# Kernel optimization log

Hardware: AMD Instinct MI355X
Metric: run time of the kernel (lower is better)

The kernel has to match this reference:

```python
import jax, jax.numpy as jnp
import numpy as np

B, NC, A, C, G = 8, 6, 25200, 10, 20  # batch, cameras, anchors, classes, GT per camera
MAX_GT = 32                            # padded GT slots per camera (>= max num_gt)
LAMBDA_COORD, LAMBDA_NOOBJ, LAMBDA_OBJ, LAMBDA_CLS = 5.0, 0.5, 1.0, 1.0
IOU_THR = 0.5


def setup_inputs() -> dict:
    key = jax.random.key(0)
    k1, k2, k3, k4, k5, k6, k7 = jax.random.split(key, 7)
    cams = B * NC
    gt_cxcy = jax.random.uniform(k1, (cams * G, 2), minval=0.1, maxval=0.9)
    gt_wh = jax.random.uniform(k2, (cams * G, 2), minval=0.05, maxval=0.3)
    gt_boxes = jnp.concatenate([gt_cxcy, gt_wh], axis=-1)           # (960, 4) cxcywh, normalized
    gt_labels = jax.random.randint(k3, (cams * G,), 0, C)            # (960,)
    # per-sample cumulative end indices: [20, 40, ..., 120] per row
    start_end_idx = jnp.tile((jnp.arange(NC) + 1) * G, (B, 1)).astype(jnp.int32)
    pred_boxes = jax.random.uniform(k4, (cams, A, 4))
    # overlay noisy copies of the GT boxes on the first G anchors so positives exist
    noise = 0.01 * jax.random.normal(k5, (cams, G, 4))
    pred_boxes = pred_boxes.at[:, :G, :].set(gt_boxes.reshape(cams, G, 4) + noise)
    pred_labels = jax.random.normal(k6, (cams, A, C))
    pred_objectness = jax.random.normal(k7, (cams, A, 1))
    return {
        'pred_boxes': pred_boxes,
        'pred_labels': pred_labels,
        'pred_objectness': pred_objectness,
        'gt_boxes': gt_boxes,
        'gt_labels': gt_labels,
        'start_end_idx': start_end_idx,
    }


def _iou_cxcywh(pb, gb):
    # pb: (cams, A, 4), gb: (cams, MG, 4) -> (cams, A, MG)
    p = pb[:, :, None, :]
    g = gb[:, None, :, :]
    p1, p2 = p[..., :2] - p[..., 2:] * 0.5, p[..., :2] + p[..., 2:] * 0.5
    g1, g2 = g[..., :2] - g[..., 2:] * 0.5, g[..., :2] + g[..., 2:] * 0.5
    wh = jnp.clip(jnp.minimum(p2, g2) - jnp.maximum(p1, g1), 0.0)
    inter = wh[..., 0] * wh[..., 1]
    area_p = p[..., 2] * p[..., 3]
    area_g = g[..., 2] * g[..., 3]
    return inter / (area_p + area_g - inter + 1e-6)


def _safe_mean(x, mask):
    # per-camera mean over masked anchors; 0 if mask empty. x, mask: (cams, A)
    cnt = mask.sum(-1)
    s = (x * mask).sum(-1)
    return jnp.where(cnt > 0, s / jnp.maximum(cnt, 1.0), 0.0)


def reference(pred_boxes, pred_labels, pred_objectness, gt_boxes, gt_labels, start_end_idx):
    cams = pred_boxes.shape[0]
    s = start_end_idx.astype(jnp.int32)                              # (B, NC) per-sample cumulative
    offsets = jnp.concatenate([jnp.zeros((1,), jnp.int32), jnp.cumsum(s[:, -1])])[:-1]  # (B,)
    starts = (offsets[:, None] + jnp.concatenate(
        [jnp.zeros((s.shape[0], 1), jnp.int32), s[:, :-1]], axis=1)).reshape(-1)        # (cams,)
    ends = (offsets[:, None] + s).reshape(-1)                        # (cams,)
    ngt = ends - starts                                              # (cams,)

    k = jnp.arange(MAX_GT, dtype=jnp.int32)
    gidx = starts[:, None] + k[None, :]                              # (cams, MG)
    valid = k[None, :] < ngt[:, None]                                # (cams, MG)
    gidx_c = jnp.clip(gidx, 0, gt_boxes.shape[0] - 1)
    gtb = gt_boxes[gidx_c]                                           # (cams, MG, 4)
    gtl = gt_labels[gidx_c]                                          # (cams, MG)

    iou = _iou_cxcywh(pred_boxes, gtb)                               # (cams, A, MG)
    iou = jnp.where(valid[:, None, :], iou, -1.0)
    best_iou = iou.max(-1)                                           # (cams, A)
    best_gt = iou.argmax(-1)                                         # (cams, A)

    has_gt = ngt > 0
    pos = ((best_iou > IOU_THR) & has_gt[:, None]).astype(pred_boxes.dtype)  # (cams, A)
    neg = 1.0 - pos
    num_pos = pos.sum()
    num_neg = neg.sum()

    cam_ix = jnp.arange(cams)[:, None]
    matched_box = gtb[cam_ix, best_gt]                               # (cams, A, 4)
    matched_lbl = gtl[cam_ix, best_gt]                               # (cams, A)

    # box loss: per-camera sum of squared errors over positives, lambda_coord weighted
    box_se = ((pred_boxes - matched_box) ** 2).sum(-1)               # (cams, A)
    box_loss_c = LAMBDA_COORD * (box_se * pos).sum(-1)               # (cams,)

    # objectness BCE-with-logits: target 1 -> softplus(-x); target 0 -> softplus(x)
    o = pred_objectness[..., 0]                                      # (cams, A)
    obj_loss_c = LAMBDA_OBJ * _safe_mean(jax.nn.softplus(-o), pos)
    noobj_loss_c = LAMBDA_NOOBJ * _safe_mean(jax.nn.softplus(o), neg)

    # classification CE over positives (per-camera mean)
    logp = jax.nn.log_softmax(pred_labels, axis=-1)                  # (cams, A, C)
    ce = -jnp.take_along_axis(logp, matched_lbl[..., None], axis=-1)[..., 0]
    cls_loss_c = LAMBDA_CLS * _safe_mean(ce, pos)

    box_loss = jnp.where(num_pos > 0, box_loss_c.sum() / jnp.maximum(num_pos, 1.0), 0.0)
    obj_loss = jnp.where(num_pos > 0, obj_loss_c.sum() / jnp.maximum(num_pos, 1.0), 0.0)
    cls_loss = jnp.where(num_pos > 0, cls_loss_c.sum() / jnp.maximum(num_pos, 1.0), 0.0)
    noobj_loss = jnp.where(num_neg > 0, noobj_loss_c.sum() / jnp.maximum(num_neg, 1.0), 0.0)
    total_loss = box_loss + obj_loss + noobj_loss + cls_loss
    return jnp.stack([total_loss, box_loss, obj_loss, noobj_loss, cls_loss])
```

## Files before the change

### kernel.cpp

```cpp
#include <hip/hip_runtime.h>
#include <math.h>

#define NCAMS 48
#define NC_   6
#define A_    25200
#define C_    10
#define MAXGT 32
#define IOU_THR 0.5f
#define L_COORD 5.0f
#define L_NOOBJ 0.5f

#define BLOCK  256
#define CHUNK  (BLOCK * 2)
#define NCHUNK ((A_ + CHUNK - 1) / CHUNK)

__device__ __forceinline__ float softplus_f(float x) {
    return fmaxf(x, 0.0f) + log1pf(expf(-fabsf(x)));
}

__global__ __launch_bounds__(BLOCK)
void yolo_phase1(const float* __restrict__ pred_boxes,
                 const float* __restrict__ pred_labels,
                 const float* __restrict__ pred_obj,
                 const float* __restrict__ gt_boxes,
                 const int*   __restrict__ gt_labels,
                 const int*   __restrict__ se,
                 int total_gt,
                 float* __restrict__ partials)
{
    const int cam   = blockIdx.y;
    const int chunk = blockIdx.x;
    const int tid   = threadIdx.x;

    __shared__ float4 s_corner[MAXGT];
    __shared__ float4 s_orig[MAXGT];
    __shared__ float  s_area[MAXGT];
    __shared__ int    s_lbl[MAXGT];
    __shared__ float  s_red[BLOCK / 64][6];

    const int b  = cam / NC_;
    const int nc = cam - b * NC_;
    int off = 0;
    for (int bb = 0; bb < b; ++bb) off += se[bb * NC_ + (NC_ - 1)];
    const int start = off + (nc ? se[b * NC_ + nc - 1] : 0);
    const int end   = off + se[b * NC_ + nc];
    int ngt = end - start;
    if (ngt < 0) ngt = 0;
    if (ngt > MAXGT) ngt = MAXGT;

    if (tid < ngt) {
        int gi = start + tid;
        gi = min(max(gi, 0), total_gt - 1);
        float4 gb = ((const float4*)gt_boxes)[gi];
        float hw = gb.z * 0.5f, hh = gb.w * 0.5f;
        s_corner[tid] = make_float4(gb.x - hw, gb.y - hh, gb.x + hw, gb.y + hh);
        s_orig[tid]   = gb;
        s_area[tid]   = gb.z * gb.w;
        s_lbl[tid]    = gt_labels[gi];
    }
    __syncthreads();

    const int base = chunk * CHUNK;
    const int a0 = base + tid;
    const int a1 = base + BLOCK + tid;
    const bool valid0 = (a0 < A_);
    const bool valid1 = (a1 < A_);
    const int a0c = valid0 ? a0 : (A_ - 1);
    const int a1c = valid1 ? a1 : (A_ - 1);
    const long long idx0 = (long long)cam * A_ + a0c;
    const long long idx1 = (long long)cam * A_ + a1c;

    const float4* pb4 = (const float4*)pred_boxes;
    const float4 p0 = pb4[idx0];
    const float4 p1 = pb4[idx1];
    const float o0 = pred_obj[idx0];
    const float o1 = pred_obj[idx1];

    const float p1x0 = p0.x - p0.z * 0.5f, p1y0 = p0.y - p0.w * 0.5f;
    const float p2x0 = p0.x + p0.z * 0.5f, p2y0 = p0.y + p0.w * 0.5f;
    const float pa0  = p0.z * p0.w + 1e-6f;
    const float p1x1 = p1.x - p1.z * 0.5f, p1y1 = p1.y - p1.w * 0.5f;
    const float p2x1 = p1.x + p1.z * 0.5f, p2y1 = p1.y + p1.w * 0.5f;
    const float pa1  = p1.z * p1.w + 1e-6f;

    float best0 = -1.0f, best1 = -1.0f;
    int bk0 = 0, bk1 = 0;

    auto iou_step = [&](int k) {
        const float4 g = s_corner[k];
        const float ga = s_area[k];
        float wx0 = fmaxf(fminf(p2x0, g.z) - fmaxf(p1x0, g.x), 0.0f);
        float wy0 = fmaxf(fminf(p2y0, g.w) - fmaxf(p1y0, g.y), 0.0f);
        float wx1 = fmaxf(fminf(p2x1, g.z) - fmaxf(p1x1, g.x), 0.0f);
        float wy1 = fmaxf(fminf(p2y1, g.w) - fmaxf(p1y1, g.y), 0.0f);
        const float inter0 = wx0 * wy0;
        const float inter1 = wx1 * wy1;
        const float iou0 = inter0 * __builtin_amdgcn_rcpf(pa0 + (ga - inter0));
        const float iou1 = inter1 * __builtin_amdgcn_rcpf(pa1 + (ga - inter1));
        if (iou0 > best0) { best0 = iou0; bk0 = k; }
        if (iou1 > best1) { best1 = iou1; bk1 = k; }
    };

    if (ngt == 20) {
        #pragma unroll
        for (int k = 0; k < 20; ++k) iou_step(k);
    } else {
        for (int k = 0; k < ngt; ++k) iou_step(k);
    }

    float pos_cnt = 0.f, neg_cnt = 0.f;
    float box_acc = 0.f, spp_acc = 0.f, spn_acc = 0.f, ce_acc = 0.f;

    auto accumulate = [&](bool valid, float best, int bk, const float4& p,
                          float o, long long idx) {
        if (!valid) return;
        if (best > IOU_THR) {
            pos_cnt += 1.0f;
            const float4 mb = s_orig[bk];
            const float dx = p.x - mb.x, dy = p.y - mb.y;
            const float dz = p.z - mb.z, dw = p.w - mb.w;
            box_acc += dx * dx + dy * dy + dz * dz + dw * dw;
            spp_acc += softplus_f(-o);
            const float* lg = pred_labels + idx * C_;
            float m = lg[0];
            #pragma unroll
            for (int i = 1; i < C_; ++i) m = fmaxf(m, lg[i]);
            float sexp = 0.f;
            #pragma unroll
            for (int i = 0; i < C_; ++i) sexp += expf(lg[i] - m);
            const int lbl = s_lbl[bk];
            ce_acc += -(lg[lbl] - m - logf(sexp));
        } else {
            neg_cnt += 1.0f;
            spn_acc += softplus_f(o);
        }
    };
    accumulate(valid0, best0, bk0, p0, o0, idx0);
    accumulate(valid1, best1, bk1, p1, o1, idx1);

    float v[6] = {pos_cnt, neg_cnt, box_acc, spp_acc, spn_acc, ce_acc};
    #pragma unroll
    for (int i = 0; i < 6; ++i) {
        float x = v[i];
        for (int s = 32; s; s >>= 1) x += __shfl_down(x, s, 64);
        v[i] = x;
    }
    if ((tid & 63) == 0) {
        const int w = tid >> 6;
        #pragma unroll
        for (int i = 0; i < 6; ++i) s_red[w][i] = v[i];
    }
    __syncthreads();
    if (tid == 0) {
        float* outp = partials + (size_t)(cam * NCHUNK + chunk) * 8;
        #pragma unroll
        for (int i = 0; i < 6; ++i)
            outp[i] = s_red[0][i] + s_red[1][i] + s_red[2][i] + s_red[3][i];
    }
}

__global__ void yolo_phase2(const float* __restrict__ partials,
                            float* __restrict__ out)
{
    const int t = threadIdx.x;
    float box_sum = 0.f, obj_sum = 0.f, noobj_sum = 0.f, cls_sum = 0.f;
    float np_ = 0.f, nn_ = 0.f;

    if (t < NCAMS) {
        float p = 0.f, n = 0.f, bx = 0.f, sp = 0.f, sn = 0.f, ce = 0.f;
        for (int h = 0; h < NCHUNK; ++h) {
            const float* q = partials + (size_t)(t * NCHUNK + h) * 8;
            p  += q[0]; n  += q[1]; bx += q[2];
            sp += q[3]; sn += q[4]; ce += q[5];
        }
        box_sum   = L_COORD * bx;
        obj_sum   = (p > 0.f) ? sp / fmaxf(p, 1.0f) : 0.f;
        cls_sum   = (p > 0.f) ? ce / fmaxf(p, 1.0f) : 0.f;
        noobj_sum = L_NOOBJ * ((n > 0.f) ? sn / fmaxf(n, 1.0f) : 0.f);
        np_ = p; nn_ = n;
    }
    for (int s = 32; s; s >>= 1) {
        box_sum   += __shfl_down(box_sum, s, 64);
        obj_sum   += __shfl_down(obj_sum, s, 64);
        noobj_sum += __shfl_down(noobj_sum, s, 64);
        cls_sum   += __shfl_down(cls_sum, s, 64);
        np_       += __shfl_down(np_, s, 64);
        nn_       += __shfl_down(nn_, s, 64);
    }
    if (t == 0) {
        const float box_loss   = (np_ > 0.f) ? box_sum / fmaxf(np_, 1.0f) : 0.f;
        const float obj_loss   = (np_ > 0.f) ? obj_sum / fmaxf(np_, 1.0f) : 0.f;
        const float cls_loss   = (np_ > 0.f) ? cls_sum / fmaxf(np_, 1.0f) : 0.f;
        const float noobj_loss = (nn_ > 0.f) ? noobj_sum / fmaxf(nn_, 1.0f) : 0.f;
        const float total = box_loss + obj_loss + noobj_loss + cls_loss;
        out[0] = total;
        out[1] = box_loss;
        out[2] = obj_loss;
        out[3] = noobj_loss;
        out[4] = cls_loss;
    }
}

extern "C" void kernel_launch(void* const* d_in, const int* in_sizes, int n_in,
                              void* d_out, int out_size, void* d_ws, size_t ws_size,
                              hipStream_t stream) {
    const float* pred_boxes  = (const float*)d_in[0];
    const float* pred_labels = (const float*)d_in[1];
    const float* pred_obj    = (const float*)d_in[2];
    const float* gt_boxes    = (const float*)d_in[3];
    const int*   gt_labels   = (const int*)d_in[4];
    const int*   se          = (const int*)d_in[5];
    const int total_gt = in_sizes[3] / 4;

    float* partials = (float*)d_ws;

    dim3 grid(NCHUNK, NCAMS);
    yolo_phase1<<<grid, BLOCK, 0, stream>>>(pred_boxes, pred_labels, pred_obj,
                                            gt_boxes, gt_labels, se,
                                            total_gt, partials);
    yolo_phase2<<<1, 64, 0, stream>>>(partials, (float*)d_out);
}
```

Baseline: 124.3 us.

## Fuse reduction kernels via last-block atomics, raise anchors per thread, drop IoU divide

Merges the two-kernel reduction into one kernel. Each block atomically adds its per-camera sums, and the last block to finish, found with an atomic counter, computes the final losses. This removes the second kernel launch and its serial partials scan, but it adds a memset launch and float atomics whose order is nondeterministic. Each thread now handles four anchors instead of two, which halves the number of blocks. The IoU argmax uses a cross-multiplied comparison instead of a reciprocal, which removes rcp instructions but may change tie and precision behaviour slightly.

```diff
diff --git a/kernel.cpp b/kernel.cpp
--- a/kernel.cpp
+++ b/kernel.cpp
@@ -6,27 +6,30 @@
 #define A_    25200
 #define C_    10
 #define MAXGT 32
-#define IOU_THR 0.5f
 #define L_COORD 5.0f
 #define L_NOOBJ 0.5f
 
 #define BLOCK  256
-#define CHUNK  (BLOCK * 2)
+#define APT    4
+#define CHUNK  (BLOCK * APT)
 #define NCHUNK ((A_ + CHUNK - 1) / CHUNK)
+#define NBLK   (NCHUNK * NCAMS)
 
 __device__ __forceinline__ float softplus_f(float x) {
     return fmaxf(x, 0.0f) + log1pf(expf(-fabsf(x)));
 }
 
 __global__ __launch_bounds__(BLOCK)
-void yolo_phase1(const float* __restrict__ pred_boxes,
-                 const float* __restrict__ pred_labels,
-                 const float* __restrict__ pred_obj,
-                 const float* __restrict__ gt_boxes,
-                 const int*   __restrict__ gt_labels,
-                 const int*   __restrict__ se,
-                 int total_gt,
-                 float* __restrict__ partials)
+void yolo_fused(const float* __restrict__ pred_boxes,
+                const float* __restrict__ pred_labels,
+                const float* __restrict__ pred_obj,
+                const float* __restrict__ gt_boxes,
+                const int*   __restrict__ gt_labels,
+                const int*   __restrict__ se,
+                int total_gt,
+                float* __restrict__ acc,
+                unsigned int* __restrict__ cnt,
+                float* __restrict__ out)
 {
     const int cam   = blockIdx.y;
     const int chunk = blockIdx.x;
@@ -37,6 +40,7 @@
     __shared__ float  s_area[MAXGT];
     __shared__ int    s_lbl[MAXGT];
     __shared__ float  s_red[BLOCK / 64][6];
+    __shared__ int    s_last;
 
     const int b  = cam / NC_;
     const int nc = cam - b * NC_;
@@ -61,44 +65,46 @@
     __syncthreads();
 
     const int base = chunk * CHUNK;
-    const int a0 = base + tid;
-    const int a1 = base + BLOCK + tid;
-    const bool valid0 = (a0 < A_);
-    const bool valid1 = (a1 < A_);
-    const int a0c = valid0 ? a0 : (A_ - 1);
-    const int a1c = valid1 ? a1 : (A_ - 1);
-    const long long idx0 = (long long)cam * A_ + a0c;
-    const long long idx1 = (long long)cam * A_ + a1c;
-
     const float4* pb4 = (const float4*)pred_boxes;
-    const float4 p0 = pb4[idx0];
-    const float4 p1 = pb4[idx1];
-    const float o0 = pred_obj[idx0];
-    const float o1 = pred_obj[idx1];
-
-    const float p1x0 = p0.x - p0.z * 0.5f, p1y0 = p0.y - p0.w * 0.5f;
-    const float p2x0 = p0.x + p0.z * 0.5f, p2y0 = p0.y + p0.w * 0.5f;
-    const float pa0  = p0.z * p0.w + 1e-6f;
-    const float p1x1 = p1.x - p1.z * 0.5f, p1y1 = p1.y - p1.w * 0.5f;
-    const float p2x1 = p1.x + p1.z * 0.5f, p2y1 = p1.y + p1.w * 0.5f;
-    const float pa1  = p1.z * p1.w + 1e-6f;
-
-    float best0 = -1.0f, best1 = -1.0f;
-    int bk0 = 0, bk1 = 0;
+
+    float4 p[APT];
+    float  o[APT];
+    float  p1x[APT], p1y[APT], p2x[APT], p2y[APT], pa[APT];
+    float  bi[APT], db[APT];
+    int    bk[APT], idx[APT];
+    bool   valid[APT];
+
+    #pragma unroll
+    for (int i = 0; i < APT; ++i) {
+        int a = base + i * BLOCK + tid;
+        valid[i] = (a < A_);
+        int ac = valid[i] ? a : (A_ - 1);
+        idx[i] = cam * A_ + ac;
+        p[i] = pb4[idx[i]];
+        o[i] = pred_obj[idx[i]];
+        p1x[i] = p[i].x - p[i].z * 0.5f;
+        p1y[i] = p[i].y - p[i].w * 0.5f;
+        p2x[i] = p[i].x + p[i].z * 0.5f;
+        p2y[i] = p[i].y + p[i].w * 0.5f;
+        pa[i]  = p[i].z * p[i].w + 1e-6f;
+        bi[i]  = -1.0f;
+        db[i]  = 1.0f;
+        bk[i]  = 0;
+    }
 
     auto iou_step = [&](int k) {
-        const float4 g = s_corner[k];
-        const float ga = s_area[k];
-        float wx0 = fmaxf(fminf(p2x0, g.z) - fmaxf(p1x0, g.x), 0.0f);
-        float wy0 = fmaxf(fminf(p2y0, g.w) - fmaxf(p1y0, g.y), 0.0f);
-        float wx1 = fmaxf(fminf(p2x1, g.z) - fmaxf(p1x1, g.x), 0.0f);
-        float wy1 = fmaxf(fminf(p2y1, g.w) - fmaxf(p1y1, g.y), 0.0f);
-        const float inter0 = wx0 * wy0;
-        const float inter1 = wx1 * wy1;
-        const float iou0 = inter0 * __builtin_amdgcn_rcpf(pa0 + (ga - inter0));
-        const float iou1 = inter1 * __builtin_amdgcn_rcpf(pa1 + (ga - inter1));
-        if (iou0 > best0) { best0 = iou0; bk0 = k; }
-        if (iou1 > best1) { best1 = iou1; bk1 = k; }
+        const float4 g  = s_corner[k];
+        const float  ga = s_area[k];
+        #pragma unroll
+        for (int i = 0; i < APT; ++i) {
+            float wx = fmaxf(fminf(p2x[i], g.z) - fmaxf(p1x[i], g.x), 0.0f);
+            float wy = fmaxf(fminf(p2y[i], g.w) - fmaxf(p1y[i], g.y), 0.0f);
+            float inter = wx * wy;
+            float den   = pa[i] + (ga - inter);
+            if (inter * db[i] > bi[i] * den) {
+                bi[i] = inter; db[i] = den; bk[i] = k;
+            }
+        }
     };
 
     if (ngt == 20) {
@@ -111,32 +117,29 @@
     float pos_cnt = 0.f, neg_cnt = 0.f;
     float box_acc = 0.f, spp_acc = 0.f, spn_acc = 0.f, ce_acc = 0.f;
 
-    auto accumulate = [&](bool valid, float best, int bk, const float4& p,
-                          float o, long long idx) {
-        if (!valid) return;
-        if (best > IOU_THR) {
+    #pragma unroll
+    for (int i = 0; i < APT; ++i) {
+        if (!valid[i]) continue;
+        if (bi[i] > 0.5f * db[i]) {
             pos_cnt += 1.0f;
-            const float4 mb = s_orig[bk];
-            const float dx = p.x - mb.x, dy = p.y - mb.y;
-            const float dz = p.z - mb.z, dw = p.w - mb.w;
+            const float4 mb = s_orig[bk[i]];
+            const float dx = p[i].x - mb.x, dy = p[i].y - mb.y;
+            const float dz = p[i].z - mb.z, dw = p[i].w - mb.w;
             box_acc += dx * dx + dy * dy + dz * dz + dw * dw;
-            spp_acc += softplus_f(-o);
-            const float* lg = pred_labels + idx * C_;
+            spp_acc += softplus_f(-o[i]);
+            const float* lg = pred_labels + (size_t)idx[i] * C_;
             float m = lg[0];
             #pragma unroll
-            for (int i = 1; i < C_; ++i) m = fmaxf(m, lg[i]);
+            for (int j = 1; j < C_; ++j) m = fmaxf(m, lg[j]);
             float sexp = 0.f;
             #pragma unroll
-            for (int i = 0; i < C_; ++i) sexp += expf(lg[i] - m);
-            const int lbl = s_lbl[bk];
-            ce_acc += -(lg[lbl] - m - logf(sexp));
+            for (int j = 0; j < C_; ++j) sexp += expf(lg[j] - m);
+            ce_acc += -(lg[s_lbl[bk[i]]] - m - logf(sexp));
         } else {
             neg_cnt += 1.0f;
-            spn_acc += softplus_f(o);
-        }
-    };
-    accumulate(valid0, best0, bk0, p0, o0, idx0);
-    accumulate(valid1, best1, bk1, p1, o1, idx1);
+            spn_acc += softplus_f(o[i]);
+        }
+    }
 
     float v[6] = {pos_cnt, neg_cnt, box_acc, spp_acc, spn_acc, ce_acc};
     #pragma unroll
@@ -151,53 +154,57 @@
         for (int i = 0; i < 6; ++i) s_red[w][i] = v[i];
     }
     __syncthreads();
+
     if (tid == 0) {
-        float* outp = partials + (size_t)(cam * NCHUNK + chunk) * 8;
-        #pragma unroll
-        for (int i = 0; i < 6; ++i)
-            outp[i] = s_red[0][i] + s_red[1][i] + s_red[2][i] + s_red[3][i];
-    }
-}
-
-__global__ void yolo_phase2(const float* __restrict__ partials,
-                            float* __restrict__ out)
-{
-    const int t = threadIdx.x;
-    float box_sum = 0.f, obj_sum = 0.f, noobj_sum = 0.f, cls_sum = 0.f;
-    float np_ = 0.f, nn_ = 0.f;
-
-    if (t < NCAMS) {
-        float p = 0.f, n = 0.f, bx = 0.f, sp = 0.f, sn = 0.f, ce = 0.f;
-        for (int h = 0; h < NCHUNK; ++h) {
-            const float* q = partials + (size_t)(t * NCHUNK + h) * 8;
-            p  += q[0]; n  += q[1]; bx += q[2];
-            sp += q[3]; sn += q[4]; ce += q[5];
-        }
-        box_sum   = L_COORD * bx;
-        obj_sum   = (p > 0.f) ? sp / fmaxf(p, 1.0f) : 0.f;
-        cls_sum   = (p > 0.f) ? ce / fmaxf(p, 1.0f) : 0.f;
-        noobj_sum = L_NOOBJ * ((n > 0.f) ? sn / fmaxf(n, 1.0f) : 0.f);
-        np_ = p; nn_ = n;
-    }
-    for (int s = 32; s; s >>= 1) {
-        box_sum   += __shfl_down(box_sum, s, 64);
-        obj_sum   += __shfl_down(obj_sum, s, 64);
-        noobj_sum += __shfl_down(noobj_sum, s, 64);
-        cls_sum   += __shfl_down(cls_sum, s, 64);
-        np_       += __shfl_down(np_, s, 64);
-        nn_       += __shfl_down(nn_, s, 64);
-    }
-    if (t == 0) {
-        const float box_loss   = (np_ > 0.f) ? box_sum / fmaxf(np_, 1.0f) : 0.f;
-        const float obj_loss   = (np_ > 0.f) ? obj_sum / fmaxf(np_, 1.0f) : 0.f;
-        const float cls_loss   = (np_ > 0.f) ? cls_sum / fmaxf(np_, 1.0f) : 0.f;
-        const float noobj_loss = (nn_ > 0.f) ? noobj_sum / fmaxf(nn_, 1.0f) : 0.f;
-        const float total = box_loss + obj_loss + noobj_loss + cls_loss;
-        out[0] = total;
-        out[1] = box_loss;
-        out[2] = obj_loss;
-        out[3] = noobj_loss;
-        out[4] = cls_loss;
+        float* a = acc + cam * 8;
+        #pragma unroll
+        for (int i = 0; i < 6; ++i) {
+            float s = s_red[0][i] + s_red[1][i] + s_red[2][i] + s_red[3][i];
+            atomicAdd(a + i, s);
+        }
+        __threadfence();
+        unsigned int old = __hip_atomic_fetch_add(
+            cnt, 1u, __ATOMIC_ACQ_REL, __HIP_MEMORY_SCOPE_AGENT);
+        s_last = (old == NBLK - 1);
+    }
+    __syncthreads();
+
+    if (s_last && tid < 64) {
+        float pC = 0.f, nC = 0.f, bxs = 0.f, objs = 0.f, noos = 0.f, clss = 0.f;
+        if (tid < NCAMS) {
+            const float* a = acc + tid * 8;
+            float pp = __hip_atomic_load(a + 0, __ATOMIC_ACQUIRE, __HIP_MEMORY_SCOPE_AGENT);
+            float nn = __hip_atomic_load(a + 1, __ATOMIC_ACQUIRE, __HIP_MEMORY_SCOPE_AGENT);
+            float bx = __hip_atomic_load(a + 2, __ATOMIC_ACQUIRE, __HIP_MEMORY_SCOPE_AGENT);
+            float sp = __hip_atomic_load(a + 3, __ATOMIC_ACQUIRE, __HIP_MEMORY_SCOPE_AGENT);
+            float sn = __hip_atomic_load(a + 4, __ATOMIC_ACQUIRE, __HIP_MEMORY_SCOPE_AGENT);
+            float ce = __hip_atomic_load(a + 5, __ATOMIC_ACQUIRE, __HIP_MEMORY_SCOPE_AGENT);
+            pC   = pp;
+            nC   = nn;
+            bxs  = L_COORD * bx;
+            objs = (pp > 0.f) ? sp / fmaxf(pp, 1.0f) : 0.f;
+            clss = (pp > 0.f) ? ce / fmaxf(pp, 1.0f) : 0.f;
+            noos = L_NOOBJ * ((nn > 0.f) ? sn / fmaxf(nn, 1.0f) : 0.f);
+        }
+        for (int s = 32; s; s >>= 1) {
+            pC   += __shfl_down(pC,   s, 64);
+            nC   += __shfl_down(nC,   s, 64);
+            bxs  += __shfl_down(bxs,  s, 64);
+            objs += __shfl_down(objs, s, 64);
+            noos += __shfl_down(noos, s, 64);
+            clss += __shfl_down(clss, s, 64);
+        }
+        if (tid == 0) {
+            const float box_loss   = (pC > 0.f) ? bxs  / fmaxf(pC, 1.f) : 0.f;
+            const float obj_loss   = (pC > 0.f) ? objs / fmaxf(pC, 1.f) : 0.f;
+            const float cls_loss   = (pC > 0.f) ? clss / fmaxf(pC, 1.f) : 0.f;
+            const float noobj_loss = (nC > 0.f) ? noos / fmaxf(nC, 1.f) : 0.f;
+            out[0] = box_loss + obj_loss + noobj_loss + cls_loss;
+            out[1] = box_loss;
+            out[2] = obj_loss;
+            out[3] = noobj_loss;
+            out[4] = cls_loss;
+        }
     }
 }
 
@@ -212,11 +219,13 @@
     const int*   se          = (const int*)d_in[5];
     const int total_gt = in_sizes[3] / 4;
 
-    float* partials = (float*)d_ws;
+    float*        acc = (float*)d_ws;
+    unsigned int* cnt = (unsigned int*)((char*)d_ws + NCAMS * 8 * sizeof(float));
+
+    hipMemsetAsync(d_ws, 0, NCAMS * 8 * sizeof(float) + 64, stream);
 
     dim3 grid(NCHUNK, NCAMS);
-    yolo_phase1<<<grid, BLOCK, 0, stream>>>(pred_boxes, pred_labels, pred_obj,
-                                            gt_boxes, gt_labels, se,
-                                            total_gt, partials);
-    yolo_phase2<<<1, 64, 0, stream>>>(partials, (float*)d_out);
+    yolo_fused<<<grid, BLOCK, 0, stream>>>(pred_boxes, pred_labels, pred_obj,
+                                           gt_boxes, gt_labels, se, total_gt,
+                                           acc, cnt, (float*)d_out);
 }
```

Measured after the change: 171.7 us. 1.38x slower.
